# Optimization experiments

Measured on AMD Instinct MI355X. Metric: run time of the kernel, lower is better.

Reference implementation:

```python
import jax, jax.numpy as jnp
import numpy as np

B, S, D, H = 4, 2048, 512, 8
HD = D // H  # head_dim = 64


def setup_inputs() -> dict:
    key = jax.random.key(0)
    ks = jax.random.split(key, 10)
    scale = 1.0 / np.sqrt(D)  # keep activations O(1)
    x = jax.random.normal(ks[0], (B, S, D), dtype=jnp.float32)
    # causal mask, broadcast over batch and heads
    causal = jnp.tril(jnp.ones((S, S), dtype=bool))
    mask = jnp.broadcast_to(causal, (B, H, S, S))
    def lin(k):
        return jax.random.normal(k, (D, D), dtype=jnp.float32) * scale
    return {
        "x": x,
        "mask": mask,
        "Wq": lin(ks[1]), "bq": jax.random.normal(ks[2], (D,), dtype=jnp.float32) * 0.01,
        "Wk": lin(ks[3]), "bk": jax.random.normal(ks[4], (D,), dtype=jnp.float32) * 0.01,
        "Wv": lin(ks[5]), "bv": jax.random.normal(ks[6], (D,), dtype=jnp.float32) * 0.01,
        "Wo": lin(ks[7]), "bo": jax.random.normal(ks[8], (D,), dtype=jnp.float32) * 0.01,
    }


def reference(x, mask, Wq, bq, Wk, bk, Wv, bv, Wo, bo):
    # eqx.nn.Linear computes W @ x + b per row; batched form is x @ W.T + b.
    b, s, d = x.shape
    q = jnp.einsum("bsd,ed->bse", x, Wq) + bq
    k = jnp.einsum("bsd,ed->bse", x, Wk) + bk
    v = jnp.einsum("bsd,ed->bse", x, Wv) + bv
    # [B, H, S, HD]
    q = q.reshape(b, s, H, HD).transpose(0, 2, 1, 3)
    k = k.reshape(b, s, H, HD).transpose(0, 2, 1, 3)
    v = v.reshape(b, s, H, HD).transpose(0, 2, 1, 3)
    scores = jnp.einsum("bhqd,bhkd->bhqk", q, k) / jnp.sqrt(jnp.asarray(HD, x.dtype))
    scores = jnp.where(mask, scores, jnp.asarray(-1e9, x.dtype))
    attn = jax.nn.softmax(scores, axis=-1)
    attended = jnp.einsum("bhqk,bhkd->bhqd", attn, v)
    attended = attended.transpose(0, 2, 1, 3).reshape(b, s, d)
    out = jnp.einsum("bsd,ed->bse", attended, Wo) + bo
    return out
```

## Files before the change

kernel.cpp:

```cpp
#include <hip/hip_runtime.h>

#define S_LEN 2048
#define DM    512
#define NH    8
#define HD    64

typedef unsigned short u16;
typedef unsigned int   u32;
typedef __bf16 bf16_t;
typedef bf16_t bf16x8 __attribute__((ext_vector_type(8)));
typedef float  f32x4  __attribute__((ext_vector_type(4)));

__device__ __forceinline__ u16 f2bf(float f) {
    u32 u = __float_as_uint(f);
    u += 0x7FFFu + ((u >> 16) & 1u);
    return (u16)(u >> 16);
}

__device__ __forceinline__ void g2l16(const u16* g, u16* l) {
    __builtin_amdgcn_global_load_lds(
        (const __attribute__((address_space(1))) u32*)g,
        (__attribute__((address_space(3))) u32*)l,
        16, 0, 0);
}

__device__ __forceinline__ float qmax16(float v) {
    v = fmaxf(v, __shfl_xor(v, 1));
    v = fmaxf(v, __shfl_xor(v, 2));
    v = fmaxf(v, __shfl_xor(v, 4));
    v = fmaxf(v, __shfl_xor(v, 8));
    return v;
}
__device__ __forceinline__ float qsum16(float v) {
    v += __shfl_xor(v, 1);
    v += __shfl_xor(v, 2);
    v += __shfl_xor(v, 4);
    v += __shfl_xor(v, 8);
    return v;
}

__global__ __launch_bounds__(256) void cvt_bf16(
    const float* __restrict__ x,
    const float* __restrict__ wq, const float* __restrict__ wk,
    const float* __restrict__ wv, const float* __restrict__ wo,
    u16* __restrict__ xb, u16* __restrict__ wqb, u16* __restrict__ wkb,
    u16* __restrict__ wvb, u16* __restrict__ wob)
{
    const int y = blockIdx.y;
    const float* src; u16* dst; int n;
    if (y == 0)      { src = x;  dst = xb;  n = 4 * S_LEN * DM; }
    else if (y == 1) { src = wq; dst = wqb; n = DM * DM; }
    else if (y == 2) { src = wk; dst = wkb; n = DM * DM; }
    else if (y == 3) { src = wv; dst = wvb; n = DM * DM; }
    else             { src = wo; dst = wob; n = DM * DM; }
    int idx = (blockIdx.x * 256 + threadIdx.x) * 8;
    if (idx >= n) return;
    float4 f0 = *(const float4*)(src + idx);
    float4 f1 = *(const float4*)(src + idx + 4);
    u32 p0 = (u32)f2bf(f0.x) | ((u32)f2bf(f0.y) << 16);
    u32 p1 = (u32)f2bf(f0.z) | ((u32)f2bf(f0.w) << 16);
    u32 p2 = (u32)f2bf(f1.x) | ((u32)f2bf(f1.y) << 16);
    u32 p3 = (u32)f2bf(f1.z) | ((u32)f2bf(f1.w) << 16);
    *(uint4*)(dst + idx) = make_uint4(p0, p1, p2, p3);
}

__global__ __launch_bounds__(256) void qkv_gemm(
    const u16* __restrict__ xb,
    const u16* __restrict__ Wqb, const u16* __restrict__ Wkb, const u16* __restrict__ Wvb,
    const float* __restrict__ bq, const float* __restrict__ bk, const float* __restrict__ bv,
    u16* __restrict__ Qb, u16* __restrict__ Kb, u16* __restrict__ Vb)
{
    __shared__ u16 Als[2][4096];
    __shared__ u16 Bls[2][4096];

    const int t = threadIdx.x;
    const int lane = t & 63, w = t >> 6;
    const int ln = lane & 15, quad = lane >> 4;
    const int wm = w >> 1, wn = w & 1;
    const int m0 = blockIdx.x * 128;
    const int mat = blockIdx.y >> 2;
    const int n0 = (blockIdx.y & 3) * 128;

    const u16* __restrict__ Wb     = (mat == 0) ? Wqb : (mat == 1) ? Wkb : Wvb;
    const float* __restrict__ bias = (mat == 0) ? bq : (mat == 1) ? bk : bv;
    u16* __restrict__ outp         = (mat == 0) ? Qb : (mat == 1) ? Kb : Vb;

    const int ch0 = (w * 2 + 0) * 64 + lane;
    const int ch1 = (w * 2 + 1) * 64 + lane;
    const int sr0 = ch0 >> 2, sk0 = (ch0 & 3) ^ ((sr0 >> 1) & 3);
    const int sr1 = ch1 >> 2, sk1 = (ch1 & 3) ^ ((sr1 >> 1) & 3);
    const u16* pA0 = xb + (size_t)(m0 + sr0) * DM + sk0 * 8;
    const u16* pA1 = xb + (size_t)(m0 + sr1) * DM + sk1 * 8;
    const u16* pB0 = Wb + (size_t)(n0 + sr0) * DM + sk0 * 8;
    const u16* pB1 = Wb + (size_t)(n0 + sr1) * DM + sk1 * 8;
    const int lo0 = (w * 2 + 0) * 512;
    const int lo1 = (w * 2 + 1) * 512;

    g2l16(pA0, &Als[0][lo0]);
    g2l16(pA1, &Als[0][lo1]);
    g2l16(pB0, &Bls[0][lo0]);
    g2l16(pB1, &Bls[0][lo1]);

    f32x4 acc[4][4] = {};
    for (int it = 0; it < 16; ++it) {
        const int cur = it & 1, nxt = cur ^ 1;
        __syncthreads();
        if (it + 1 < 16) {
            const int k0n = (it + 1) * 32;
            g2l16(pA0 + k0n, &Als[nxt][lo0]);
            g2l16(pA1 + k0n, &Als[nxt][lo1]);
            g2l16(pB0 + k0n, &Bls[nxt][lo0]);
            g2l16(pB1 + k0n, &Bls[nxt][lo1]);
        }
        bf16x8 af[4], bf8[4];
        #pragma unroll
        for (int i = 0; i < 4; ++i) {
            int row = wm * 64 + i * 16 + ln;
            af[i] = *(const bf16x8*)(&Als[cur][0] + (row * 4 + (quad ^ ((row >> 1) & 3))) * 8);
        }
        #pragma unroll
        for (int j = 0; j < 4; ++j) {
            int row = wn * 64 + j * 16 + ln;
            bf8[j] = *(const bf16x8*)(&Bls[cur][0] + (row * 4 + (quad ^ ((row >> 1) & 3))) * 8);
        }
        #pragma unroll
        for (int i = 0; i < 4; ++i)
            #pragma unroll
            for (int j = 0; j < 4; ++j)
                acc[i][j] = __builtin_amdgcn_mfma_f32_16x16x32_bf16(af[i], bf8[j], acc[i][j], 0, 0, 0);
    }

    #pragma unroll
    for (int j = 0; j < 4; ++j) {
        int colg = n0 + wn * 64 + j * 16 + ln;
        float bj = bias[colg];
        int h = colg >> 6, d = colg & 63;
        #pragma unroll
        for (int i = 0; i < 4; ++i) {
            int mbase = m0 + wm * 64 + i * 16 + quad * 4;
            #pragma unroll
            for (int r = 0; r < 4; ++r) {
                int m = mbase + r;
                int bb = m >> 11, s = m & 2047;
                outp[(((size_t)bb * NH + h) * S_LEN + s) * HD + d] = f2bf(acc[i][j][r] + bj);
            }
        }
    }
}

__global__ __launch_bounds__(256) void attn_mfma(
    const u16* __restrict__ Qb, const u16* __restrict__ Kb, const u16* __restrict__ Vb,
    u16* __restrict__ Attb)
{
    __shared__ u16 Qls[4096];
    __shared__ u16 Kls[2][4096];
    __shared__ u16 Vt[2][4096];
    __shared__ u16 Ps[4096];

    const int t = threadIdx.x;
    const int lane = t & 63, w = t >> 6;
    const int ln = lane & 15, quad = lane >> 4;
    const int bh = blockIdx.y;
    const int qt = (blockIdx.x + bh) & 31;
    const int q_base = qt * 64;
    const size_t base = (size_t)bh * S_LEN * HD;

    const int c0 = (w * 2 + 0) * 64 + lane;
    const int c1 = (w * 2 + 1) * 64 + lane;
    const int r0 = c0 >> 3, k0s = (c0 & 7) ^ (r0 & 7);
    const int r1 = c1 >> 3, k1s = (c1 & 7) ^ (r1 & 7);
    const int lo0 = (w * 2 + 0) * 512;
    const int lo1 = (w * 2 + 1) * 512;

    g2l16(Qb + base + (size_t)(q_base + r0) * HD + k0s * 8, Qls + lo0);
    g2l16(Qb + base + (size_t)(q_base + r1) * HD + k1s * 8, Qls + lo1);

    const u16* pK0 = Kb + base + (size_t)r0 * HD + k0s * 8;
    const u16* pK1 = Kb + base + (size_t)r1 * HD + k1s * 8;
    g2l16(pK0, &Kls[0][lo0]);
    g2l16(pK1, &Kls[0][lo1]);

    const int vkey0 = t >> 3, vd0 = (t & 7) * 8;
    const int vkey1 = (t + 256) >> 3;
    const u16* pV0 = Vb + base + (size_t)vkey0 * HD + vd0;
    const u16* pV1 = Vb + base + (size_t)vkey1 * HD + vd0;
    const int kvq0 = vkey0 >> 3, kvl0 = vkey0 & 7;
    const int kvq1 = vkey1 >> 3, kvl1 = vkey1 & 7;

    {
        uint4 vv0 = *(const uint4*)(pV0);
        uint4 vv1 = *(const uint4*)(pV1);
        u16 ve[8];
        *(uint4*)ve = vv0;
        #pragma unroll
        for (int ii = 0; ii < 8; ++ii) {
            int i = (ii + (t & 7)) & 7;
            int d = vd0 + i;
            Vt[0][(d * 8 + (kvq0 ^ (d & 7))) * 8 + kvl0] = ve[i];
        }
        *(uint4*)ve = vv1;
        #pragma unroll
        for (int ii = 0; ii < 8; ++ii) {
            int i = (ii + (t & 7)) & 7;
            int d = vd0 + i;
            Vt[0][(d * 8 + (kvq1 ^ (d & 7))) * 8 + kvl1] = ve[i];
        }
    }
    __syncthreads();

    bf16x8 aq[2];
    #pragma unroll
    for (int ks = 0; ks < 2; ++ks) {
        int row = w * 16 + ln;
        aq[ks] = *(const bf16x8*)(Qls + (row * 8 + ((ks * 4 + quad) ^ (row & 7))) * 8);
    }

    float m_st[4], l_st[4], alpha[4];
    f32x4 o[4] = {};
    #pragma unroll
    for (int r = 0; r < 4; ++r) { m_st[r] = -1e30f; l_st[r] = 0.f; }

    const float sc = 0.125f * 1.44269504f;
    const int qrow_base = q_base + w * 16;

    for (int kt = 0; kt <= qt; ++kt) {
        const int cur = kt & 1, nxt = cur ^ 1;
        __syncthreads();

        uint4 vv0, vv1;
        const bool more = (kt < qt);
        if (more) {
            const size_t off = (size_t)(kt + 1) * 64 * HD;
            g2l16(pK0 + off, &Kls[nxt][lo0]);
            g2l16(pK1 + off, &Kls[nxt][lo1]);
            vv0 = *(const uint4*)(pV0 + off);
            vv1 = *(const uint4*)(pV1 + off);
        }

        f32x4 s[4] = {};
        #pragma unroll
        for (int ks = 0; ks < 2; ++ks)
            #pragma unroll
            for (int j = 0; j < 4; ++j) {
                int krow = j * 16 + ln;
                bf16x8 bk8 = *(const bf16x8*)(&Kls[cur][0] + (krow * 8 + ((ks * 4 + quad) ^ (krow & 7))) * 8);
                s[j] = __builtin_amdgcn_mfma_f32_16x16x32_bf16(aq[ks], bk8, s[j], 0, 0, 0);
            }

        if (more) {
            u16 ve[8];
            *(uint4*)ve = vv0;
            #pragma unroll
            for (int ii = 0; ii < 8; ++ii) {
                int i = (ii + (t & 7)) & 7;
                int d = vd0 + i;
                Vt[nxt][(d * 8 + (kvq0 ^ (d & 7))) * 8 + kvl0] = ve[i];
            }
            *(uint4*)ve = vv1;
            #pragma unroll
            for (int ii = 0; ii < 8; ++ii) {
                int i = (ii + (t & 7)) & 7;
                int d = vd0 + i;
                Vt[nxt][(d * 8 + (kvq1 ^ (d & 7))) * 8 + kvl1] = ve[i];
            }
        }

        if (kt == qt) {
            #pragma unroll
            for (int j = 0; j < 4; ++j)
                #pragma unroll
                for (int r = 0; r < 4; ++r) {
                    int qg = qrow_base + quad * 4 + r;
                    int kg = kt * 64 + j * 16 + ln;
                    s[j][r] = (kg > qg) ? -1e30f : s[j][r] * sc;
                }
        } else {
            #pragma unroll
            for (int j = 0; j < 4; ++j)
                #pragma unroll
                for (int r = 0; r < 4; ++r)
                    s[j][r] *= sc;
        }

        #pragma unroll
        for (int r = 0; r < 4; ++r) {
            float mx = fmaxf(fmaxf(s[0][r], s[1][r]), fmaxf(s[2][r], s[3][r]));
            mx = qmax16(mx);
            float mnew = fmaxf(m_st[r], mx);
            float al = __builtin_amdgcn_exp2f(m_st[r] - mnew);
            m_st[r] = mnew;
            float rs = 0.f;
            #pragma unroll
            for (int j = 0; j < 4; ++j) {
                float p = __builtin_amdgcn_exp2f(s[j][r] - mnew);
                s[j][r] = p;
                rs += p;
            }
            rs = qsum16(rs);
            l_st[r] = l_st[r] * al + rs;
            alpha[r] = al;
        }
        #pragma unroll
        for (int j = 0; j < 4; ++j)
            #pragma unroll
            for (int r = 0; r < 4; ++r)
                o[j][r] *= alpha[r];

        #pragma unroll
        for (int j = 0; j < 4; ++j) {
            int key = j * 16 + ln;
            int kq = key >> 3, kl = key & 7;
            #pragma unroll
            for (int r = 0; r < 4; ++r) {
                int qrow = w * 16 + quad * 4 + r;
                Ps[(qrow * 8 + (kq ^ (qrow & 7))) * 8 + kl] = f2bf(s[j][r]);
            }
        }

        #pragma unroll
        for (int ks = 0; ks < 2; ++ks) {
            int kqg = ks * 4 + quad;
            int prow = w * 16 + ln;
            bf16x8 pa = *(const bf16x8*)(Ps + (prow * 8 + (kqg ^ (prow & 7))) * 8);
            #pragma unroll
            for (int j = 0; j < 4; ++j) {
                int rowd = j * 16 + ln;
                bf16x8 vb8 = *(const bf16x8*)(&Vt[cur][0] + (rowd * 8 + (kqg ^ (rowd & 7))) * 8);
                o[j] = __builtin_amdgcn_mfma_f32_16x16x32_bf16(pa, vb8, o[j], 0, 0, 0);
            }
        }
    }

    const int bb = bh >> 3, h = bh & 7;
    #pragma unroll
    for (int r = 0; r < 4; ++r) {
        int qg = q_base + w * 16 + quad * 4 + r;
        float inv = 1.f / l_st[r];
        #pragma unroll
        for (int j = 0; j < 4; ++j) {
            int d = j * 16 + ln;
            Attb[((size_t)(bb * S_LEN + qg)) * DM + h * HD + d] = f2bf(o[j][r] * inv);
        }
    }
}

__global__ __launch_bounds__(256) void out_gemm(
    const u16* __restrict__ Ab, const u16* __restrict__ Wob,
    const float* __restrict__ bo, float* __restrict__ out)
{
    __shared__ u16 Als[2][4096];
    __shared__ u16 Bls[2][4096];

    const int t = threadIdx.x;
    const int lane = t & 63, w = t >> 6;
    const int ln = lane & 15, quad = lane >> 4;
    const int wm = w >> 1, wn = w & 1;
    const int m0 = blockIdx.x * 128;
    const int n0 = blockIdx.y * 128;

    const int ch0 = (w * 2 + 0) * 64 + lane;
    const int ch1 = (w * 2 + 1) * 64 + lane;
    const int sr0 = ch0 >> 2, sk0 = (ch0 & 3) ^ ((sr0 >> 1) & 3);
    const int sr1 = ch1 >> 2, sk1 = (ch1 & 3) ^ ((sr1 >> 1) & 3);
    const u16* pA0 = Ab  + (size_t)(m0 + sr0) * DM + sk0 * 8;
    const u16* pA1 = Ab  + (size_t)(m0 + sr1) * DM + sk1 * 8;
    const u16* pB0 = Wob + (size_t)(n0 + sr0) * DM + sk0 * 8;
    const u16* pB1 = Wob + (size_t)(n0 + sr1) * DM + sk1 * 8;
    const int lo0 = (w * 2 + 0) * 512;
    const int lo1 = (w * 2 + 1) * 512;

    g2l16(pA0, &Als[0][lo0]);
    g2l16(pA1, &Als[0][lo1]);
    g2l16(pB0, &Bls[0][lo0]);
    g2l16(pB1, &Bls[0][lo1]);

    f32x4 acc[4][4] = {};
    for (int it = 0; it < 16; ++it) {
        const int cur = it & 1, nxt = cur ^ 1;
        __syncthreads();
        if (it + 1 < 16) {
            const int k0n = (it + 1) * 32;
            g2l16(pA0 + k0n, &Als[nxt][lo0]);
            g2l16(pA1 + k0n, &Als[nxt][lo1]);
            g2l16(pB0 + k0n, &Bls[nxt][lo0]);
            g2l16(pB1 + k0n, &Bls[nxt][lo1]);
        }
        bf16x8 af[4], bf8[4];
        #pragma unroll
        for (int i = 0; i < 4; ++i) {
            int row = wm * 64 + i * 16 + ln;
            af[i] = *(const bf16x8*)(&Als[cur][0] + (row * 4 + (quad ^ ((row >> 1) & 3))) * 8);
        }
        #pragma unroll
        for (int j = 0; j < 4; ++j) {
            int row = wn * 64 + j * 16 + ln;
            bf8[j] = *(const bf16x8*)(&Bls[cur][0] + (row * 4 + (quad ^ ((row >> 1) & 3))) * 8);
        }
        #pragma unroll
        for (int i = 0; i < 4; ++i)
            #pragma unroll
            for (int j = 0; j < 4; ++j)
                acc[i][j] = __builtin_amdgcn_mfma_f32_16x16x32_bf16(af[i], bf8[j], acc[i][j], 0, 0, 0);
    }

    #pragma unroll
    for (int j = 0; j < 4; ++j) {
        int colg = n0 + wn * 64 + j * 16 + ln;
        float bj = bo[colg];
        #pragma unroll
        for (int i = 0; i < 4; ++i) {
            int mbase = m0 + wm * 64 + i * 16 + quad * 4;
            #pragma unroll
            for (int r = 0; r < 4; ++r) {
                int m = mbase + r;
                out[(size_t)m * DM + colg] = acc[i][j][r] + bj;
            }
        }
    }
}

extern "C" void kernel_launch(void* const* d_in, const int* in_sizes, int n_in,
                              void* d_out, int out_size, void* d_ws, size_t ws_size,
                              hipStream_t stream) {
    const float* x  = (const float*)d_in[0];
    const float* Wq = (const float*)d_in[2];
    const float* bq = (const float*)d_in[3];
    const float* Wk = (const float*)d_in[4];
    const float* bk = (const float*)d_in[5];
    const float* Wv = (const float*)d_in[6];
    const float* bv = (const float*)d_in[7];
    const float* Wo = (const float*)d_in[8];
    const float* bo = (const float*)d_in[9];
    float* out = (float*)d_out;

    u16* ws = (u16*)d_ws;
    const size_t NX = (size_t)4 * S_LEN * DM;
    const size_t NW = (size_t)DM * DM;
    u16* xb   = ws;
    u16* wqb  = xb + NX;
    u16* wkb  = wqb + NW;
    u16* wvb  = wkb + NW;
    u16* wob  = wvb + NW;
    u16* Qb   = wob + NW;
    u16* Kb   = Qb + NX;
    u16* Vb   = Kb + NX;
    u16* Attb = Vb + NX;

    cvt_bf16<<<dim3(2048, 5), 256, 0, stream>>>(x, Wq, Wk, Wv, Wo, xb, wqb, wkb, wvb, wob);
    qkv_gemm<<<dim3(64, 12), 256, 0, stream>>>(xb, wqb, wkb, wvb, bq, bk, bv, Qb, Kb, Vb);
    attn_mfma<<<dim3(32, 32), 256, 0, stream>>>(Qb, Kb, Vb, Attb);
    out_gemm<<<dim3(64, 4), 256, 0, stream>>>(Attb, wob, bo, out);
}
```

Baseline: 751.6 us.

## Fold softmax scale into Q, add lazy rescaling, MFMA priority, smaller out-GEMM tiles

Folds the 1/sqrt(HD)*log2(e) softmax scale into the Q projection epilogue, which removes the per-tile score multiply in attention. Adds conditional online-softmax rescaling that skips the alpha rescale of O when the row max has not grown by more than 8 (in log2 units). Wraps the MFMA sections in s_setprio to favour matrix issue. Shrinks the output GEMM M-tile to 64 so twice as many blocks run. The lazy rescale lets exponentials exceed 1 (up to 2^8) before renormalisation, which can cost bf16 accuracy in P.

Result: slower. 769.6 us (+2.4%).

```diff
diff --git a/kernel.cpp b/kernel.cpp
--- a/kernel.cpp
+++ b/kernel.cpp
@@ -84,6 +84,7 @@
     const u16* __restrict__ Wb     = (mat == 0) ? Wqb : (mat == 1) ? Wkb : Wvb;
     const float* __restrict__ bias = (mat == 0) ? bq : (mat == 1) ? bk : bv;
     u16* __restrict__ outp         = (mat == 0) ? Qb : (mat == 1) ? Kb : Vb;
+    const float qscale             = (mat == 0) ? 0.18033688f : 1.0f;
 
     const int ch0 = (w * 2 + 0) * 64 + lane;
     const int ch1 = (w * 2 + 1) * 64 + lane;
@@ -142,7 +143,7 @@
             for (int r = 0; r < 4; ++r) {
                 int m = mbase + r;
                 int bb = m >> 11, s = m & 2047;
-                outp[(((size_t)bb * NH + h) * S_LEN + s) * HD + d] = f2bf(acc[i][j][r] + bj);
+                outp[(((size_t)bb * NH + h) * S_LEN + s) * HD + d] = f2bf((acc[i][j][r] + bj) * qscale);
             }
         }
     }
@@ -220,7 +221,6 @@
     #pragma unroll
     for (int r = 0; r < 4; ++r) { m_st[r] = -1e30f; l_st[r] = 0.f; }
 
-    const float sc = 0.125f * 1.44269504f;
     const int qrow_base = q_base + w * 16;
 
     for (int kt = 0; kt <= qt; ++kt) {
@@ -238,6 +238,7 @@
         }
 
         f32x4 s[4] = {};
+        __builtin_amdgcn_s_setprio(1);
         #pragma unroll
         for (int ks = 0; ks < 2; ++ks)
             #pragma unroll
@@ -246,6 +247,7 @@
                 bf16x8 bk8 = *(const bf16x8*)(&Kls[cur][0] + (krow * 8 + ((ks * 4 + quad) ^ (krow & 7))) * 8);
                 s[j] = __builtin_amdgcn_mfma_f32_16x16x32_bf16(aq[ks], bk8, s[j], 0, 0, 0);
             }
+        __builtin_amdgcn_s_setprio(0);
 
         if (more) {
             u16 ve[8];
@@ -272,39 +274,54 @@
                 for (int r = 0; r < 4; ++r) {
                     int qg = qrow_base + quad * 4 + r;
                     int kg = kt * 64 + j * 16 + ln;
-                    s[j][r] = (kg > qg) ? -1e30f : s[j][r] * sc;
+                    if (kg > qg) s[j][r] = -1e30f;
                 }
-        } else {
+        }
+
+        float mx[4];
+        #pragma unroll
+        for (int r = 0; r < 4; ++r) {
+            float v = fmaxf(fmaxf(s[0][r], s[1][r]), fmaxf(s[2][r], s[3][r]));
+            mx[r] = qmax16(v);
+        }
+        bool grow = (mx[0] > m_st[0] + 8.f) || (mx[1] > m_st[1] + 8.f) ||
+                    (mx[2] > m_st[2] + 8.f) || (mx[3] > m_st[3] + 8.f);
+        if (__any((int)grow)) {
+            #pragma unroll
+            for (int r = 0; r < 4; ++r) {
+                float mnew = fmaxf(m_st[r], mx[r]);
+                float al = __builtin_amdgcn_exp2f(m_st[r] - mnew);
+                m_st[r] = mnew;
+                float rs = 0.f;
+                #pragma unroll
+                for (int j = 0; j < 4; ++j) {
+                    float p = __builtin_amdgcn_exp2f(s[j][r] - mnew);
+                    s[j][r] = p;
+                    rs += p;
+                }
+                rs = qsum16(rs);
+                l_st[r] = l_st[r] * al + rs;
+                alpha[r] = al;
+            }
             #pragma unroll
             for (int j = 0; j < 4; ++j)
                 #pragma unroll
                 for (int r = 0; r < 4; ++r)
-                    s[j][r] *= sc;
-        }
-
-        #pragma unroll
-        for (int r = 0; r < 4; ++r) {
-            float mx = fmaxf(fmaxf(s[0][r], s[1][r]), fmaxf(s[2][r], s[3][r]));
-            mx = qmax16(mx);
-            float mnew = fmaxf(m_st[r], mx);
-            float al = __builtin_amdgcn_exp2f(m_st[r] - mnew);
-            m_st[r] = mnew;
-            float rs = 0.f;
-            #pragma unroll
-            for (int j = 0; j < 4; ++j) {
-                float p = __builtin_amdgcn_exp2f(s[j][r] - mnew);
-                s[j][r] = p;
-                rs += p;
-            }
-            rs = qsum16(rs);
-            l_st[r] = l_st[r] * al + rs;
-            alpha[r] = al;
-        }
-        #pragma unroll
-        for (int j = 0; j < 4; ++j)
-            #pragma unroll
-            for (int r = 0; r < 4; ++r)
-                o[j][r] *= alpha[r];
+                    o[j][r] *= alpha[r];
+        } else {
+            #pragma unroll
+            for (int r = 0; r < 4; ++r) {
+                float rs = 0.f;
+                #pragma unroll
+                for (int j = 0; j < 4; ++j) {
+                    float p = __builtin_amdgcn_exp2f(s[j][r] - m_st[r]);
+                    s[j][r] = p;
+                    rs += p;
+                }
+                rs = qsum16(rs);
+                l_st[r] += rs;
+            }
+        }
 
         #pragma unroll
         for (int j = 0; j < 4; ++j) {
@@ -317,6 +334,7 @@
             }
         }
 
+        __builtin_amdgcn_s_setprio(1);
         #pragma unroll
         for (int ks = 0; ks < 2; ++ks) {
             int kqg = ks * 4 + quad;
@@ -329,6 +347,7 @@
                 o[j] = __builtin_amdgcn_mfma_f32_16x16x32_bf16(pa, vb8, o[j], 0, 0, 0);
             }
         }
+        __builtin_amdgcn_s_setprio(0);
     }
 
     const int bb = bh >> 3, h = bh & 7;
@@ -348,68 +367,68 @@
     const u16* __restrict__ Ab, const u16* __restrict__ Wob,
     const float* __restrict__ bo, float* __restrict__ out)
 {
-    __shared__ u16 Als[2][4096];
+    __shared__ u16 Als[2][2048];
     __shared__ u16 Bls[2][4096];
 
     const int t = threadIdx.x;
     const int lane = t & 63, w = t >> 6;
     const int ln = lane & 15, quad = lane >> 4;
-    const int wm = w >> 1, wn = w & 1;
-    const int m0 = blockIdx.x * 128;
+    const int m0 = blockIdx.x * 64;
     const int n0 = blockIdx.y * 128;
+
+    const int cha = w * 64 + lane;
+    const int sra = cha >> 2, ska = (cha & 3) ^ ((sra >> 1) & 3);
+    const u16* pA = Ab + (size_t)(m0 + sra) * DM + ska * 8;
+    const int loa = w * 512;
 
     const int ch0 = (w * 2 + 0) * 64 + lane;
     const int ch1 = (w * 2 + 1) * 64 + lane;
     const int sr0 = ch0 >> 2, sk0 = (ch0 & 3) ^ ((sr0 >> 1) & 3);
     const int sr1 = ch1 >> 2, sk1 = (ch1 & 3) ^ ((sr1 >> 1) & 3);
-    const u16* pA0 = Ab  + (size_t)(m0 + sr0) * DM + sk0 * 8;
-    const u16* pA1 = Ab  + (size_t)(m0 + sr1) * DM + sk1 * 8;
     const u16* pB0 = Wob + (size_t)(n0 + sr0) * DM + sk0 * 8;
     const u16* pB1 = Wob + (size_t)(n0 + sr1) * DM + sk1 * 8;
     const int lo0 = (w * 2 + 0) * 512;
     const int lo1 = (w * 2 + 1) * 512;
 
-    g2l16(pA0, &Als[0][lo0]);
-    g2l16(pA1, &Als[0][lo1]);
+    g2l16(pA,  &Als[0][loa]);
     g2l16(pB0, &Bls[0][lo0]);
     g2l16(pB1, &Bls[0][lo1]);
 
-    f32x4 acc[4][4] = {};
+    f32x4 acc[4][2] = {};
     for (int it = 0; it < 16; ++it) {
         const int cur = it & 1, nxt = cur ^ 1;
         __syncthreads();
         if (it + 1 < 16) {
             const int k0n = (it + 1) * 32;
-            g2l16(pA0 + k0n, &Als[nxt][lo0]);
-            g2l16(pA1 + k0n, &Als[nxt][lo1]);
+            g2l16(pA + k0n,  &Als[nxt][loa]);
             g2l16(pB0 + k0n, &Bls[nxt][lo0]);
             g2l16(pB1 + k0n, &Bls[nxt][lo1]);
         }
-        bf16x8 af[4], bf8[4];
+        bf16x8 af[4], bf8[2];
         #pragma unroll
         for (int i = 0; i < 4; ++i) {
-            int row = wm * 64 + i * 16 + ln;
+            int row = i * 16 + ln;
             af[i] = *(const bf16x8*)(&Als[cur][0] + (row * 4 + (quad ^ ((row >> 1) & 3))) * 8);
         }
         #pragma unroll
-        for (int j = 0; j < 4; ++j) {
-            int row = wn * 64 + j * 16 + ln;
+        for (int j = 0; j < 2; ++j) {
+            int row = w * 32 + j * 16 + ln;
             bf8[j] = *(const bf16x8*)(&Bls[cur][0] + (row * 4 + (quad ^ ((row >> 1) & 3))) * 8);
         }
         #pragma unroll
         for (int i = 0; i < 4; ++i)
             #pragma unroll
-            for (int j = 0; j < 4; ++j)
+            for (int j = 0; j < 2; ++j)
                 acc[i][j] = __builtin_amdgcn_mfma_f32_16x16x32_bf16(af[i], bf8[j], acc[i][j], 0, 0, 0);
     }
 
     #pragma unroll
-    for (int j = 0; j < 4; ++j) {
-        int colg = n0 + wn * 64 + j * 16 + ln;
+    for (int j = 0; j < 2; ++j) {
+        int colg = n0 + w * 32 + j * 16 + ln;
         float bj = bo[colg];
         #pragma unroll
         for (int i = 0; i < 4; ++i) {
-            int mbase = m0 + wm * 64 + i * 16 + quad * 4;
+            int mbase = m0 + i * 16 + quad * 4;
             #pragma unroll
             for (int r = 0; r < 4; ++r) {
                 int m = mbase + r;
@@ -449,5 +468,5 @@
     cvt_bf16<<<dim3(2048, 5), 256, 0, stream>>>(x, Wq, Wk, Wv, Wo, xb, wqb, wkb, wvb, wob);
     qkv_gemm<<<dim3(64, 12), 256, 0, stream>>>(xb, wqb, wkb, wvb, bq, bk, bv, Qb, Kb, Vb);
     attn_mfma<<<dim3(32, 32), 256, 0, stream>>>(Qb, Kb, Vb, Attb);
-    out_gemm<<<dim3(64, 4), 256, 0, stream>>>(Attb, wob, bo, out);
-}
+    out_gemm<<<dim3(128, 4), 256, 0, stream>>>(Attb, wob, bo, out);
+}
```
